# Kernel optimization log

Hardware: AMD Instinct MI355X
Metric: run time of the kernel (lower is better)

The kernel has to match this reference:

```python
import jax, jax.numpy as jnp
import numpy as np

N, E, D, H = 50000, 800000, 128, 4
DH = D // H
BN_EPS = 1e-5


def setup_inputs() -> dict:
    key = jax.random.key(0)
    ks = jax.random.split(key, 16)
    s = 0.02
    inp = {
        "x": jax.random.normal(ks[0], (N, D), dtype=jnp.float32),
        "edge_index": jax.random.randint(ks[1], (2, E), 0, N, dtype=jnp.int64),
        "Wk": jax.random.normal(ks[2], (D, D), dtype=jnp.float32) * s,
        "bk": jnp.zeros((D,), jnp.float32),
        "Wm": jax.random.normal(ks[3], (D, D), dtype=jnp.float32) * s,
        "bm": jnp.zeros((D,), jnp.float32),
        "Wq": jax.random.normal(ks[4], (D, D), dtype=jnp.float32) * s,
        "bq": jnp.zeros((D,), jnp.float32),
        "W1": jax.random.normal(ks[5], (D, D), dtype=jnp.float32) * s,
        "b1": jnp.zeros((D,), jnp.float32),
        "gamma": jnp.ones((D,), jnp.float32),
        "beta": jnp.zeros((D,), jnp.float32),
        "W2": jax.random.normal(ks[6], (D, D), dtype=jnp.float32) * s,
        "b2": jnp.zeros((D,), jnp.float32),
    }
    return inp


def reference(x, edge_index, Wk, bk, Wm, bm, Wq, bq, W1, b1, gamma, beta, W2, b2):
    src = edge_index[0]  # [E] softmax segment key
    dst = edge_index[1]  # [E] aggregation target
    x_i = x[dst]         # [E, D] (torch code: X[1])
    x_j = x[src]         # [E, D] (torch code: X[0])

    key = (x_i @ Wk + bk).reshape(-1, H, DH)
    msg = (x_j @ Wm + bm).reshape(-1, H, DH)
    query = (x_j @ Wq + bq).reshape(-1, H, DH) / jnp.sqrt(jnp.float32(DH))

    scores = jnp.sum(query * key, axis=2)  # [E, H]

    # segment softmax over src node index (numerically stable)
    smax = jax.ops.segment_max(scores, src, num_segments=N)
    e = jnp.exp(scores - smax[src])
    ssum = jax.ops.segment_sum(e, src, num_segments=N)
    alpha = e / ssum[src]  # [E, H]

    # rescale by per-src-node edge count
    cnt = jax.ops.segment_sum(jnp.ones((scores.shape[0],), jnp.float32), src, num_segments=N)
    alpha = alpha * cnt[src][:, None]

    out_e = (msg * alpha[:, :, None]).reshape(-1, D)  # [E, D]
    out = jax.ops.segment_sum(out_e, dst, num_segments=N)  # [N, D]

    # MLP: Linear -> BatchNorm1d (training-mode batch stats) -> ReLU -> Linear
    h = out @ W1 + b1
    mean = jnp.mean(h, axis=0)
    var = jnp.var(h, axis=0)  # biased variance, as torch BN uses for normalization
    h = (h - mean) * jax.lax.rsqrt(var + BN_EPS) * gamma + beta
    h = jax.nn.relu(h)
    return h @ W2 + b2
```

## Files before the change

kernel.cpp:

```cpp
#include <hip/hip_runtime.h>
#include <hip/hip_bf16.h>

#define N_NODES 50000
#define N_EDGES 800000
#define DIM 128
#define NHEAD 4
#define GEMM_BLOCKS 782
#define HBLOCKS 313
#define EPB 2560
#define NBUCK 196
#define NBUCK2 392
#define NODE_PAD 50432

typedef __bf16 bf16x8 __attribute__((ext_vector_type(8)));
typedef float f32x4 __attribute__((ext_vector_type(4)));

struct WPtrs { const float* w[5]; };

__global__ __launch_bounds__(256) void prep_weights(WPtrs P, __bf16* __restrict__ Wt)
{
  __shared__ __bf16 tileT[16][136];
  const int mat = blockIdx.x >> 3, sl = blockIdx.x & 7;
  const float* W = P.w[mat];
  const int col0 = sl * 16;
  const int t = threadIdx.x;
  #pragma unroll
  for (int i = 0; i < 8; ++i) {
    int id = t + i * 256;
    int k = id >> 4, c = id & 15;
    tileT[c][k] = (__bf16)W[k * 128 + col0 + c];
  }
  __syncthreads();
  int c = t >> 4, kb = t & 15;
  bf16x8 v = *(const bf16x8*)&tileT[c][kb * 8];
  *(bf16x8*)&Wt[(size_t)mat * 16384 + (size_t)(col0 + c) * 128 + kb * 8] = v;
}


__device__ __forceinline__ void stage_Wt_half(const __bf16* __restrict__ Wt,
    int half, __bf16 (*wLDS)[136])
{
  const int t = threadIdx.x;
  const __bf16* base = Wt + (size_t)half * 64 * 128;
  #pragma unroll
  for (int i = 0; i < 4; ++i) {
    int id = t + i * 256;
    int col = id >> 4, kb = id & 15;
    bf16x8 v = ((const bf16x8*)(base + (size_t)col * 128))[kb];
    *(bf16x8*)&wLDS[col][kb * 8] = v;
  }
}

__device__ __forceinline__ void stage_A_f32(const float* __restrict__ A, int row0,
    int nrows, __bf16 (*aLDS)[136])
{
  const int t = threadIdx.x;
  #pragma unroll
  for (int i = 0; i < 4; ++i) {
    int id = t + i * 256;
    int r = id >> 4, cb = id & 15;
    int gr = row0 + r;
    float4 v0 = make_float4(0.f, 0.f, 0.f, 0.f), v1 = v0;
    if (gr < nrows) {
      const float4* row = (const float4*)(A + (size_t)gr * DIM);
      v0 = row[cb * 2];
      v1 = row[cb * 2 + 1];
    }
    bf16x8 o;
    o[0] = (__bf16)v0.x; o[1] = (__bf16)v0.y; o[2] = (__bf16)v0.z; o[3] = (__bf16)v0.w;
    o[4] = (__bf16)v1.x; o[5] = (__bf16)v1.y; o[6] = (__bf16)v1.z; o[7] = (__bf16)v1.w;
    *(bf16x8*)&aLDS[r][cb * 8] = o;
  }
}

__device__ __forceinline__ void stage_A_bf16(const __bf16* __restrict__ A, int row0,
    int nrows, __bf16 (*aLDS)[136])
{
  const int t = threadIdx.x;
  #pragma unroll
  for (int i = 0; i < 4; ++i) {
    int id = t + i * 256;
    int r = id >> 4, cb = id & 15;
    int gr = row0 + r;
    bf16x8 v = {};
    if (gr < nrows) v = ((const bf16x8*)(A + (size_t)gr * DIM))[cb];
    *(bf16x8*)&aLDS[r][cb * 8] = v;
  }
}

__device__ __forceinline__ void mfma_half(const __bf16 (*aLDS)[136],
    const __bf16 (*wLDS)[136], int half, f32x4 acc[8])
{
  const int lane = threadIdx.x & 63, wave = threadIdx.x >> 6;
  const int m = lane & 15, q = lane >> 4;
  #pragma unroll
  for (int kt = 0; kt < 4; ++kt) {
    bf16x8 a = *(const bf16x8*)&aLDS[wave * 16 + m][kt * 32 + q * 8];
    #pragma unroll
    for (int ct = 0; ct < 4; ++ct) {
      bf16x8 b = *(const bf16x8*)&wLDS[ct * 16 + m][kt * 32 + q * 8];
      acc[half * 4 + ct] =
          __builtin_amdgcn_mfma_f32_16x16x32_bf16(a, b, acc[half * 4 + ct], 0, 0, 0);
    }
  }
}

template <typename OutT>
__device__ __forceinline__ void store_tile(f32x4 acc[8],
    const float* __restrict__ bias, float scale, OutT* __restrict__ C,
    int row0, int nrows)
{
  const int lane = threadIdx.x & 63, wave = threadIdx.x >> 6;
  const int m = lane & 15, q = lane >> 4;
  #pragma unroll
  for (int j = 0; j < 8; ++j) {
    int col = (j >> 2) * 64 + (j & 3) * 16 + m;
    float bv = bias[col];
    #pragma unroll
    for (int r = 0; r < 4; ++r) {
      int row = row0 + wave * 16 + q * 4 + r;
      if (row < nrows) C[(size_t)row * DIM + col] = (OutT)((acc[j][r] + bv) * scale);
    }
  }
}

__device__ __forceinline__ void gemm_pass(const __bf16 (*aLDS)[136],
    __bf16 (*wLDS)[136], const __bf16* __restrict__ Wt, f32x4 acc[8])
{
  #pragma unroll
  for (int i = 0; i < 8; ++i) acc[i] = (f32x4){0.f, 0.f, 0.f, 0.f};
  stage_Wt_half(Wt, 0, wLDS);
  __syncthreads();
  mfma_half(aLDS, wLDS, 0, acc);
  __syncthreads();
  stage_Wt_half(Wt, 1, wLDS);
  __syncthreads();
  mfma_half(aLDS, wLDS, 1, acc);
}

__global__ __launch_bounds__(256) void fat1(const int* __restrict__ ei,
    int* __restrict__ hist,
    const __bf16* __restrict__ Wt, const float* __restrict__ x,
    const float* __restrict__ bk, const float* __restrict__ bm,
    const float* __restrict__ bq,
    __bf16* __restrict__ Kn, __bf16* __restrict__ Mn, __bf16* __restrict__ Qn)
{
  __shared__ __bf16 aLDS[64][136];
  __shared__ __bf16 wLDS[64][136];
  const int b = blockIdx.x, t = threadIdx.x;

  if (b < HBLOCKS) {
    int* h = (int*)&aLDS[0][0];
    for (int i = t; i < NBUCK2; i += 256) h[i] = 0;
    __syncthreads();
    #pragma unroll
    for (int i = 0; i < 10; ++i) {
      int e = b * EPB + i * 256 + t;
      if (e < N_EDGES) {
        int s = ei[e], d = ei[N_EDGES + e];
        atomicAdd(&h[s >> 8], 1);
        atomicAdd(&h[NBUCK + (d >> 8)], 1);
      }
    }
    __syncthreads();
    for (int i = t; i < NBUCK2; i += 256) hist[b * NBUCK2 + i] = h[i];
  } else {
    const int gb = b - HBLOCKS;
    const int mat = gb % 3;
    const int row0 = (gb / 3) * 64;
    const float* bias = (mat == 0) ? bk : (mat == 1) ? bm : bq;
    __bf16* out = (mat == 0) ? Kn : (mat == 1) ? Mn : Qn;
    const float scale = (mat == 2) ? 0.17677669529663689f : 1.0f;
    f32x4 acc[8];
    stage_A_f32(x, row0, N_NODES, aLDS);
    gemm_pass(aLDS, wLDS, Wt + (size_t)mat * 16384, acc);
    store_tile<__bf16>(acc, bias, scale, out, row0, N_NODES);
  }
}

__global__ __launch_bounds__(64) void bucket_scan(const int* __restrict__ hist,
    int* __restrict__ bbase, int* __restrict__ tot)
{
  const int b = blockIdx.x, l = threadIdx.x;
  int run = 0;
  for (int c = 0; c < 5; ++c) {
    int idx = c * 64 + l;
    int v = (idx < HBLOCKS) ? hist[idx * NBUCK2 + b] : 0;
    int orig = v;
    #pragma unroll
    for (int o = 1; o < 64; o <<= 1) {
      int n = __shfl_up(v, o);
      if (l >= o) v += n;
    }
    if (idx < HBLOCKS) bbase[idx * NBUCK2 + b] = run + v - orig;
    run += __shfl(v, 63);
  }
  if (l == 0) tot[b] = run;
}

__global__ __launch_bounds__(256) void bucket_starts(const int* __restrict__ tot,
    int* __restrict__ bstart)
{
  __shared__ int s[256];
  const int t = threadIdx.x;
  int v = (t < NBUCK) ? tot[t] : 0;
  s[t] = v; __syncthreads();
  for (int o = 1; o < 256; o <<= 1) {
    int x = (t >= o) ? s[t - o] : 0; __syncthreads();
    s[t] += x; __syncthreads();
  }
  if (t < NBUCK) bstart[t] = s[t] - v;
  __syncthreads();
  v = (t < NBUCK) ? tot[NBUCK + t] : 0;
  s[t] = v; __syncthreads();
  for (int o = 1; o < 256; o <<= 1) {
    int x = (t >= o) ? s[t - o] : 0; __syncthreads();
    s[t] += x; __syncthreads();
  }
  if (t < NBUCK) bstart[NBUCK + t] = s[t] - v;
}

__global__ __launch_bounds__(256) void edge_scatter(const int* __restrict__ ei,
    const int* __restrict__ bbase, const int* __restrict__ bstart,
    int2* __restrict__ bucketedS, int* __restrict__ bucketedD)
{
  __shared__ int base[NBUCK2];
  __shared__ int cur[NBUCK2];
  const int b = blockIdx.x, t = threadIdx.x;
  for (int i = t; i < NBUCK2; i += 256) {
    base[i] = bstart[i] + bbase[b * NBUCK2 + i];
    cur[i] = 0;
  }
  __syncthreads();
  #pragma unroll
  for (int i = 0; i < 10; ++i) {
    int e = b * EPB + i * 256 + t;
    if (e < N_EDGES) {
      int s = ei[e], d = ei[N_EDGES + e];
      int pk = s | (d << 16);
      int bs = s >> 8, bd = NBUCK + (d >> 8);
      int lo = atomicAdd(&cur[bs], 1);
      int ld = atomicAdd(&cur[bd], 1);
      int slotD = base[bd] + ld;
      bucketedS[base[bs] + lo] = make_int2(pk, slotD);
      bucketedD[slotD] = pk;
    }
  }
}

__global__ __launch_bounds__(256) void bucket_rank(const int2* __restrict__ bucketedS,
    const int* __restrict__ bucketedD, const int* __restrict__ bstart,
    const int* __restrict__ tot,
    int2* __restrict__ elistS, int* __restrict__ elistD,
    int* __restrict__ starts, int* __restrict__ deg,
    int* __restrict__ startsD, int* __restrict__ degD)
{
  __shared__ int c1[256], ns[256], c2[256];
  const int b = blockIdx.x, t = threadIdx.x;
  const bool srcSide = (b < NBUCK);
  const int bb = srcSide ? b : b - NBUCK;
  const int seg0 = bstart[b];
  const int cnt = tot[b];

  c1[t] = 0; c2[t] = 0;
  __syncthreads();
  if (srcSide) {
    const int2* ent = bucketedS + seg0;
    for (int i = t; i < cnt; i += 256)
      atomicAdd(&c1[(int)((unsigned)ent[i].x & 0xFFFFu) - (bb << 8)], 1);
  } else {
    const int* ent = bucketedD + seg0;
    for (int i = t; i < cnt; i += 256)
      atomicAdd(&c1[(int)((unsigned)ent[i] >> 16) - (bb << 8)], 1);
  }
  __syncthreads();
  ns[t] = c1[t]; __syncthreads();
  for (int o = 1; o < 256; o <<= 1) {
    int x = (t >= o) ? ns[t - o] : 0; __syncthreads();
    ns[t] += x; __syncthreads();
  }
  {
    int node = (bb << 8) + t;
    int st = seg0 + ns[t] - c1[t];
    if (srcSide) { starts[node] = st; deg[node] = c1[t]; }
    else         { startsD[node] = st; degD[node] = c1[t]; }
  }
  __syncthreads();
  ns[t] -= c1[t];
  __syncthreads();
  if (srcSide) {
    const int2* ent = bucketedS + seg0;
    for (int i = t; i < cnt; i += 256) {
      int2 en = ent[i];
      unsigned pk = (unsigned)en.x;
      int ln = (int)(pk & 0xFFFFu) - (bb << 8);
      int r = atomicAdd(&c2[ln], 1);
      elistS[seg0 + ns[ln] + r] = make_int2((int)(pk >> 16), en.y);
    }
  } else {
    const int* ent = bucketedD + seg0;
    for (int i = t; i < cnt; i += 256) {
      unsigned pk = (unsigned)ent[i];
      int ln = (int)(pk >> 16) - (bb << 8);
      int r = atomicAdd(&c2[ln], 1);
      elistD[seg0 + ns[ln] + r] = (int)(pk & 0xFFFFu) | (i << 16);
    }
  }
}

__global__ __launch_bounds__(256) void src_scores(const int* __restrict__ starts,
    const int* __restrict__ degS, const int2* __restrict__ elistS,
    const __bf16* __restrict__ Qn, const __bf16* __restrict__ Kn,
    float* __restrict__ wexp, float* __restrict__ factor)
{
  const int wave = threadIdx.x >> 6, l = threadIdx.x & 63;
  const int n = blockIdx.x * 4 + wave;
  const int g = l >> 4, il = l & 15;
  const int h = il >> 2;
  const int beg = starts[n], end = beg + degS[n];
  if (beg == end) return;

  bf16x8 q8 = ((const bf16x8*)(Qn + (size_t)n * DIM))[il];
  float wsum = 0.f;

  for (int p0 = beg; p0 < end; p0 += 16) {
    int pp[4]; int2 en[4];
    #pragma unroll
    for (int u = 0; u < 4; ++u) {
      pp[u] = p0 + u * 4 + g;
      en[u] = elistS[min(pp[u], end - 1)];
    }
    bf16x8 kk[4];
    #pragma unroll
    for (int u = 0; u < 4; ++u)
      kk[u] = ((const bf16x8*)(Kn + (size_t)en[u].x * DIM))[il];
    #pragma unroll
    for (int u = 0; u < 4; ++u) {
      float pr = 0.f;
      #pragma unroll
      for (int j = 0; j < 8; ++j) pr += (float)q8[j] * (float)kk[u][j];
      pr += __shfl_xor(pr, 1);
      pr += __shfl_xor(pr, 2);
      float w = (pp[u] < end) ? __expf(pr) : 0.f;
      wsum += w;
      if ((pp[u] < end) && (il & 3) == 0) wexp[(size_t)en[u].y * NHEAD + h] = w;
    }
  }
  wsum += __shfl_xor(wsum, 16);
  wsum += __shfl_xor(wsum, 32);
  if (g == 0 && (il & 3) == 0)
    factor[(size_t)n * NHEAD + h] = (float)(end - beg) / wsum;
}

__global__ __launch_bounds__(256) void dst_aggregate(const int* __restrict__ startsD,
    const int* __restrict__ degD, const int* __restrict__ elistD,
    const int* __restrict__ bstart,
    const __bf16* __restrict__ Mn, const float* __restrict__ wexp,
    const float* __restrict__ factor, __bf16* __restrict__ agg)
{
  const int wave = threadIdx.x >> 6, l = threadIdx.x & 63;
  const int n = blockIdx.x * 4 + wave;
  const int g = l >> 4, il = l & 15;
  const int h = il >> 2;
  const int beg = startsD[n], end = beg + degD[n];
  const int seg0d = bstart[NBUCK + (n >> 8)];

  float acc[8];
  #pragma unroll
  for (int j = 0; j < 8; ++j) acc[j] = 0.f;

  for (int q0 = beg; q0 < end; q0 += 16) {
    int qq[4], ss[4]; float ww[4];
    #pragma unroll
    for (int u = 0; u < 4; ++u) {
      qq[u] = q0 + u * 4 + g;
      int cq = min(qq[u], end - 1);
      int v = elistD[cq];
      ss[u] = v & 0xFFFF;
      ww[u] = wexp[(size_t)(seg0d + ((unsigned)v >> 16)) * NHEAD + h];
    }
    float ff[4];
    #pragma unroll
    for (int u = 0; u < 4; ++u) ff[u] = factor[(size_t)ss[u] * NHEAD + h];
    bf16x8 mm[4];
    #pragma unroll
    for (int u = 0; u < 4; ++u)
      mm[u] = ((const bf16x8*)(Mn + (size_t)ss[u] * DIM))[il];
    #pragma unroll
    for (int u = 0; u < 4; ++u) {
      float av = (qq[u] < end) ? ww[u] * ff[u] : 0.f;
      #pragma unroll
      for (int j = 0; j < 8; ++j) acc[j] += (float)mm[u][j] * av;
    }
  }
  #pragma unroll
  for (int j = 0; j < 8; ++j) {
    acc[j] += __shfl_xor(acc[j], 16);
    acc[j] += __shfl_xor(acc[j], 32);
  }
  if (g == 0) {
    bf16x8 o;
    #pragma unroll
    for (int j = 0; j < 8; ++j) o[j] = (__bf16)acc[j];
    *(bf16x8*)(agg + (size_t)n * DIM + il * 8) = o;
  }
}

__global__ __launch_bounds__(256) void gemm_stats(const __bf16* __restrict__ A,
    const __bf16* __restrict__ Wt, const float* __restrict__ bias,
    __bf16* __restrict__ C, float* __restrict__ colsum, float* __restrict__ colsq)
{
  __shared__ __bf16 aLDS[64][136];
  __shared__ __bf16 wLDS[64][136];
  __shared__ float csum[128], csq[128];
  const int t = threadIdx.x;
  const int row0 = blockIdx.x * 64;

  stage_A_bf16(A, row0, N_NODES, aLDS);
  if (t < 128) { csum[t] = 0.f; csq[t] = 0.f; }
  f32x4 acc[8];
  gemm_pass(aLDS, wLDS, Wt, acc);

  const int lane = t & 63, wave = t >> 6;
  const int m = lane & 15, q = lane >> 4;
  #pragma unroll
  for (int j = 0; j < 8; ++j) {
    int col = (j >> 2) * 64 + (j & 3) * 16 + m;
    float bv = bias[col];
    float s = 0.f, s2 = 0.f;
    #pragma unroll
    for (int r = 0; r < 4; ++r) {
      int row = row0 + wave * 16 + q * 4 + r;
      float hv = acc[j][r] + bv;
      if (row < N_NODES) {
        C[(size_t)row * DIM + col] = (__bf16)hv;
        s += hv; s2 += hv * hv;
      }
    }
    s  += __shfl_xor(s, 16);  s  += __shfl_xor(s, 32);
    s2 += __shfl_xor(s2, 16); s2 += __shfl_xor(s2, 32);
    if (q == 0) {
      atomicAdd(&csum[col], s);
      atomicAdd(&csq[col], s2);
    }
  }
  __syncthreads();
  if (t < 128) {
    atomicAdd(&colsum[t], csum[t]);
    atomicAdd(&colsq[t], csq[t]);
  }
}

__global__ __launch_bounds__(256) void gemm_bn(const __bf16* __restrict__ A,
    const __bf16* __restrict__ Wt, const float* __restrict__ bias,
    float* __restrict__ C, const float* __restrict__ colsum,
    const float* __restrict__ colsq, const float* __restrict__ gamma,
    const float* __restrict__ beta)
{
  __shared__ __bf16 aLDS[64][136];
  __shared__ __bf16 wLDS[64][136];
  __shared__ float sA[128], sB[128];
  const int t = threadIdx.x;
  const int row0 = blockIdx.x * 64;

  if (t < 128) {
    float mean = colsum[t] * (1.0f / N_NODES);
    float var = colsq[t] * (1.0f / N_NODES) - mean * mean;
    float inv = rsqrtf(var + 1e-5f);
    float a = gamma[t] * inv;
    sA[t] = a;
    sB[t] = beta[t] - mean * a;
  }
  __syncthreads();

  {
    const int cb = t & 15;
    float sa[8], sb[8];
    #pragma unroll
    for (int j = 0; j < 8; ++j) { sa[j] = sA[cb * 8 + j]; sb[j] = sB[cb * 8 + j]; }
    #pragma unroll
    for (int i = 0; i < 4; ++i) {
      int id = t + i * 256;
      int r = id >> 4;
      int gr = row0 + r;
      bf16x8 v = {};
      if (gr < N_NODES) v = ((const bf16x8*)(A + (size_t)gr * DIM))[cb];
      bf16x8 o;
      #pragma unroll
      for (int j = 0; j < 8; ++j)
        o[j] = (__bf16)fmaxf((float)v[j] * sa[j] + sb[j], 0.f);
      *(bf16x8*)&aLDS[r][cb * 8] = o;
    }
  }
  f32x4 acc[8];
  gemm_pass(aLDS, wLDS, Wt, acc);
  store_tile<float>(acc, bias, 1.0f, C, row0, N_NODES);
}

extern "C" void kernel_launch(void* const* d_in, const int* in_sizes, int n_in,
                              void* d_out, int out_size, void* d_ws, size_t ws_size,
                              hipStream_t stream) {
  const float* x     = (const float*)d_in[0];
  const int*   ei    = (const int*)d_in[1];
  const float* Wk    = (const float*)d_in[2];
  const float* bk    = (const float*)d_in[3];
  const float* Wm    = (const float*)d_in[4];
  const float* bm    = (const float*)d_in[5];
  const float* Wq    = (const float*)d_in[6];
  const float* bq    = (const float*)d_in[7];
  const float* W1    = (const float*)d_in[8];
  const float* b1    = (const float*)d_in[9];
  const float* gamma = (const float*)d_in[10];
  const float* beta  = (const float*)d_in[11];
  const float* W2    = (const float*)d_in[12];
  const float* b2    = (const float*)d_in[13];

  float* ws = (float*)d_ws;
  const size_t ND  = (size_t)N_NODES * DIM;
  const size_t NDh = ND / 2;
  const size_t EH  = (size_t)N_EDGES * NHEAD;

  __bf16* Kn   = (__bf16*)ws;
  __bf16* Mn   = (__bf16*)(ws + NDh);
  __bf16* Qn   = (__bf16*)(ws + 2 * NDh);
  __bf16* agg  = (__bf16*)(ws + 3 * NDh);
  __bf16* h1   = (__bf16*)(ws + 4 * NDh);
  float*  wexp = ws + 5 * NDh;
  int2*   bucketedS = (int2*)wexp;
  int*    bucketedD = (int*)(bucketedS + N_EDGES);
  int2*   elistS = (int2*)(wexp + EH);
  int*    elistD = (int*)(elistS + N_EDGES);
  int*    hist   = elistD + N_EDGES;
  int*    bbase  = hist + HBLOCKS * NBUCK2;
  int*    tot    = bbase + HBLOCKS * NBUCK2;
  int*    bstart = tot + NBUCK2;
  int*    starts = bstart + NBUCK2;
  int*    deg    = starts + NODE_PAD;
  int*    startsD= deg + NODE_PAD;
  int*    degD   = startsD + NODE_PAD;
  float*  factor = (float*)(degD + NODE_PAD);
  float*  colsum = factor + (size_t)NHEAD * N_NODES;
  float*  colsq  = colsum + 128;
  __bf16* Wt     = (__bf16*)(colsq + 128);
  float*  outp   = (float*)d_out;

  hipMemsetAsync(colsum, 0, 256 * sizeof(float), stream);

  const int node_blocks = N_NODES / 4;

  WPtrs wp; wp.w[0] = Wk; wp.w[1] = Wm; wp.w[2] = Wq; wp.w[3] = W1; wp.w[4] = W2;
  prep_weights<<<40, 256, 0, stream>>>(wp, Wt);

  fat1<<<HBLOCKS + 3 * GEMM_BLOCKS, 256, 0, stream>>>(
      ei, hist, Wt, x, bk, bm, bq, Kn, Mn, Qn);

  bucket_scan<<<NBUCK2, 64, 0, stream>>>(hist, bbase, tot);
  bucket_starts<<<1, 256, 0, stream>>>(tot, bstart);
  edge_scatter<<<HBLOCKS, 256, 0, stream>>>(ei, bbase, bstart, bucketedS, bucketedD);
  bucket_rank<<<NBUCK2, 256, 0, stream>>>(bucketedS, bucketedD, bstart, tot,
                                          elistS, elistD, starts, deg,
                                          startsD, degD);

  src_scores<<<node_blocks, 256, 0, stream>>>(starts, deg, elistS, Qn, Kn,
                                              wexp, factor);
  dst_aggregate<<<node_blocks, 256, 0, stream>>>(startsD, degD, elistD, bstart,
                                                 Mn, wexp, factor, agg);

  gemm_stats<<<GEMM_BLOCKS, 256, 0, stream>>>(agg, Wt + 3 * 16384, b1, h1,
                                              colsum, colsq);
  gemm_bn<<<GEMM_BLOCKS, 256, 0, stream>>>(h1, Wt + 4 * 16384, b2, outp,
                                           colsum, colsq, gamma, beta);
}
```

Baseline: 290.8 us.

## Store K/M/Q and agg head-major and assign one wave per node-head

```diff
diff --git a/kernel.cpp b/kernel.cpp
--- a/kernel.cpp
+++ b/kernel.cpp
@@ -5,6 +5,7 @@
 #define N_EDGES 800000
 #define DIM 128
 #define NHEAD 4
+#define HN (N_NODES * 32)
 #define GEMM_BLOCKS 782
 #define HBLOCKS 313
 #define EPB 2560
@@ -73,7 +74,7 @@
   }
 }
 
-__device__ __forceinline__ void stage_A_bf16(const __bf16* __restrict__ A, int row0,
+__device__ __forceinline__ void stage_A_hm(const __bf16* __restrict__ A, int row0,
     int nrows, __bf16 (*aLDS)[136])
 {
   const int t = threadIdx.x;
@@ -83,7 +84,8 @@
     int r = id >> 4, cb = id & 15;
     int gr = row0 + r;
     bf16x8 v = {};
-    if (gr < nrows) v = ((const bf16x8*)(A + (size_t)gr * DIM))[cb];
+    if (gr < nrows)
+      v = *(const bf16x8*)(A + (size_t)(cb >> 2) * HN + (size_t)gr * 32 + (cb & 3) * 8);
     *(bf16x8*)&aLDS[r][cb * 8] = v;
   }
 }
@@ -120,6 +122,25 @@
     for (int r = 0; r < 4; ++r) {
       int row = row0 + wave * 16 + q * 4 + r;
       if (row < nrows) C[(size_t)row * DIM + col] = (OutT)((acc[j][r] + bv) * scale);
+    }
+  }
+}
+
+__device__ __forceinline__ void store_tile_hm(f32x4 acc[8],
+    const float* __restrict__ bias, float scale, __bf16* __restrict__ C,
+    int row0, int nrows)
+{
+  const int lane = threadIdx.x & 63, wave = threadIdx.x >> 6;
+  const int m = lane & 15, q = lane >> 4;
+  #pragma unroll
+  for (int j = 0; j < 8; ++j) {
+    int col = (j >> 2) * 64 + (j & 3) * 16 + m;
+    float bv = bias[col];
+    __bf16* base = C + (size_t)(col >> 5) * HN + (col & 31);
+    #pragma unroll
+    for (int r = 0; r < 4; ++r) {
+      int row = row0 + wave * 16 + q * 4 + r;
+      if (row < nrows) base[(size_t)row * 32] = (__bf16)((acc[j][r] + bv) * scale);
     }
   }
 }
@@ -174,7 +195,7 @@
     f32x4 acc[8];
     stage_A_f32(x, row0, N_NODES, aLDS);
     gemm_pass(aLDS, wLDS, Wt + (size_t)mat * 16384, acc);
-    store_tile<__bf16>(acc, bias, scale, out, row0, N_NODES);
+    store_tile_hm(acc, bias, scale, out, row0, N_NODES);
   }
 }
 
@@ -310,91 +331,74 @@
 
 __global__ __launch_bounds__(256) void src_scores(const int* __restrict__ starts,
     const int* __restrict__ degS, const int2* __restrict__ elistS,
-    const __bf16* __restrict__ Qn, const __bf16* __restrict__ Kn,
+    const __bf16* __restrict__ Qh, const __bf16* __restrict__ Kh,
     float* __restrict__ wexp, float* __restrict__ factor)
 {
-  const int wave = threadIdx.x >> 6, l = threadIdx.x & 63;
-  const int n = blockIdx.x * 4 + wave;
-  const int g = l >> 4, il = l & 15;
-  const int h = il >> 2;
+  const int wid = blockIdx.x * 4 + (threadIdx.x >> 6);
+  const int l = threadIdx.x & 63;
+  const int n = wid >> 2, h = wid & 3;
+  const int g = l >> 2, il = l & 3;
   const int beg = starts[n], end = beg + degS[n];
   if (beg == end) return;
 
-  bf16x8 q8 = ((const bf16x8*)(Qn + (size_t)n * DIM))[il];
+  const __bf16* Kb = Kh + (size_t)h * HN;
+  bf16x8 q8 = ((const bf16x8*)(Qh + (size_t)h * HN + (size_t)n * 32))[il];
   float wsum = 0.f;
 
   for (int p0 = beg; p0 < end; p0 += 16) {
-    int pp[4]; int2 en[4];
-    #pragma unroll
-    for (int u = 0; u < 4; ++u) {
-      pp[u] = p0 + u * 4 + g;
-      en[u] = elistS[min(pp[u], end - 1)];
-    }
-    bf16x8 kk[4];
-    #pragma unroll
-    for (int u = 0; u < 4; ++u)
-      kk[u] = ((const bf16x8*)(Kn + (size_t)en[u].x * DIM))[il];
-    #pragma unroll
-    for (int u = 0; u < 4; ++u) {
-      float pr = 0.f;
-      #pragma unroll
-      for (int j = 0; j < 8; ++j) pr += (float)q8[j] * (float)kk[u][j];
-      pr += __shfl_xor(pr, 1);
-      pr += __shfl_xor(pr, 2);
-      float w = (pp[u] < end) ? __expf(pr) : 0.f;
-      wsum += w;
-      if ((pp[u] < end) && (il & 3) == 0) wexp[(size_t)en[u].y * NHEAD + h] = w;
-    }
-  }
+    int p = p0 + g;
+    int2 en = elistS[min(p, end - 1)];
+    bf16x8 kk = ((const bf16x8*)(Kb + (size_t)en.x * 32))[il];
+    float pr = 0.f;
+    #pragma unroll
+    for (int j = 0; j < 8; ++j) pr += (float)q8[j] * (float)kk[j];
+    pr += __shfl_xor(pr, 1);
+    pr += __shfl_xor(pr, 2);
+    float w = (p < end) ? __expf(pr) : 0.f;
+    wsum += w;
+    if ((p < end) && il == 0) wexp[(size_t)en.y * NHEAD + h] = w;
+  }
+  wsum += __shfl_xor(wsum, 4);
+  wsum += __shfl_xor(wsum, 8);
   wsum += __shfl_xor(wsum, 16);
   wsum += __shfl_xor(wsum, 32);
-  if (g == 0 && (il & 3) == 0)
-    factor[(size_t)n * NHEAD + h] = (float)(end - beg) / wsum;
+  if (l == 0) factor[(size_t)n * NHEAD + h] = (float)(end - beg) / wsum;
 }
 
 __global__ __launch_bounds__(256) void dst_aggregate(const int* __restrict__ startsD,
     const int* __restrict__ degD, const int* __restrict__ elistD,
     const int* __restrict__ bstart,
-    const __bf16* __restrict__ Mn, const float* __restrict__ wexp,
+    const __bf16* __restrict__ Mh, const float* __restrict__ wexp,
     const float* __restrict__ factor, __bf16* __restrict__ agg)
 {
-  const int wave = threadIdx.x >> 6, l = threadIdx.x & 63;
-  const int n = blockIdx.x * 4 + wave;
-  const int g = l >> 4, il = l & 15;
-  const int h = il >> 2;
+  const int wid = blockIdx.x * 4 + (threadIdx.x >> 6);
+  const int l = threadIdx.x & 63;
+  const int n = wid >> 2, h = wid & 3;
+  const int g = l >> 2, il = l & 3;
   const int beg = startsD[n], end = beg + degD[n];
   const int seg0d = bstart[NBUCK + (n >> 8)];
+  const __bf16* Mb = Mh + (size_t)h * HN;
 
   float acc[8];
   #pragma unroll
   for (int j = 0; j < 8; ++j) acc[j] = 0.f;
 
-  for (int q0 = beg; q0 < end; q0 += 16) {
-    int qq[4], ss[4]; float ww[4];
-    #pragma unroll
-    for (int u = 0; u < 4; ++u) {
-      qq[u] = q0 + u * 4 + g;
-      int cq = min(qq[u], end - 1);
-      int v = elistD[cq];
-      ss[u] = v & 0xFFFF;
-      ww[u] = wexp[(size_t)(seg0d + ((unsigned)v >> 16)) * NHEAD + h];
-    }
-    float ff[4];
-    #pragma unroll
-    for (int u = 0; u < 4; ++u) ff[u] = factor[(size_t)ss[u] * NHEAD + h];
-    bf16x8 mm[4];
-    #pragma unroll
-    for (int u = 0; u < 4; ++u)
-      mm[u] = ((const bf16x8*)(Mn + (size_t)ss[u] * DIM))[il];
-    #pragma unroll
-    for (int u = 0; u < 4; ++u) {
-      float av = (qq[u] < end) ? ww[u] * ff[u] : 0.f;
-      #pragma unroll
-      for (int j = 0; j < 8; ++j) acc[j] += (float)mm[u][j] * av;
-    }
+  for (int p0 = beg; p0 < end; p0 += 16) {
+    int p = p0 + g;
+    int cq = min(p, end - 1);
+    int v = elistD[cq];
+    int src = v & 0xFFFF;
+    float w = wexp[(size_t)(seg0d + ((unsigned)v >> 16)) * NHEAD + h]
+            * factor[src * NHEAD + h];
+    bf16x8 mm = ((const bf16x8*)(Mb + (size_t)src * 32))[il];
+    float av = (p < end) ? w : 0.f;
+    #pragma unroll
+    for (int j = 0; j < 8; ++j) acc[j] += (float)mm[j] * av;
   }
   #pragma unroll
   for (int j = 0; j < 8; ++j) {
+    acc[j] += __shfl_xor(acc[j], 4);
+    acc[j] += __shfl_xor(acc[j], 8);
     acc[j] += __shfl_xor(acc[j], 16);
     acc[j] += __shfl_xor(acc[j], 32);
   }
@@ -402,7 +406,7 @@
     bf16x8 o;
     #pragma unroll
     for (int j = 0; j < 8; ++j) o[j] = (__bf16)acc[j];
-    *(bf16x8*)(agg + (size_t)n * DIM + il * 8) = o;
+    *(bf16x8*)(agg + (size_t)h * HN + (size_t)n * 32 + il * 8) = o;
   }
 }
 
@@ -416,7 +420,7 @@
   const int t = threadIdx.x;
   const int row0 = blockIdx.x * 64;
 
-  stage_A_bf16(A, row0, N_NODES, aLDS);
+  stage_A_hm(A, row0, N_NODES, aLDS);
   if (t < 128) { csum[t] = 0.f; csq[t] = 0.f; }
   f32x4 acc[8];
   gemm_pass(aLDS, wLDS, Wt, acc);
@@ -546,7 +550,7 @@
 
   hipMemsetAsync(colsum, 0, 256 * sizeof(float), stream);
 
-  const int node_blocks = N_NODES / 4;
+  const int nh_blocks = N_NODES;
 
   WPtrs wp; wp.w[0] = Wk; wp.w[1] = Wm; wp.w[2] = Wq; wp.w[3] = W1; wp.w[4] = W2;
   prep_weights<<<40, 256, 0, stream>>>(wp, Wt);
@@ -561,10 +565,10 @@
                                           elistS, elistD, starts, deg,
                                           startsD, degD);
 
-  src_scores<<<node_blocks, 256, 0, stream>>>(starts, deg, elistS, Qn, Kn,
-                                              wexp, factor);
-  dst_aggregate<<<node_blocks, 256, 0, stream>>>(startsD, degD, elistD, bstart,
-                                                 Mn, wexp, factor, agg);
+  src_scores<<<nh_blocks, 256, 0, stream>>>(starts, deg, elistS, Qn, Kn,
+                                            wexp, factor);
+  dst_aggregate<<<nh_blocks, 256, 0, stream>>>(startsD, degD, elistD, bstart,
+                                               Mn, wexp, factor, agg);
 
   gemm_stats<<<GEMM_BLOCKS, 256, 0, stream>>>(agg, Wt + 3 * 16384, b1, h1,
                                               colsum, colsq);
```

Measured after the change: 367.8 us. 26.5% more time.

## Read GEMM weights directly from global memory and fuse K/M/Q projections per tile

Applied to the files above, without the earlier changes.

```diff
diff --git a/kernel.cpp b/kernel.cpp
--- a/kernel.cpp
+++ b/kernel.cpp
@@ -37,20 +37,6 @@
 }
 
 
-__device__ __forceinline__ void stage_Wt_half(const __bf16* __restrict__ Wt,
-    int half, __bf16 (*wLDS)[136])
-{
-  const int t = threadIdx.x;
-  const __bf16* base = Wt + (size_t)half * 64 * 128;
-  #pragma unroll
-  for (int i = 0; i < 4; ++i) {
-    int id = t + i * 256;
-    int col = id >> 4, kb = id & 15;
-    bf16x8 v = ((const bf16x8*)(base + (size_t)col * 128))[kb];
-    *(bf16x8*)&wLDS[col][kb * 8] = v;
-  }
-}
-
 __device__ __forceinline__ void stage_A_f32(const float* __restrict__ A, int row0,
     int nrows, __bf16 (*aLDS)[136])
 {
@@ -88,19 +74,21 @@
   }
 }
 
-__device__ __forceinline__ void mfma_half(const __bf16 (*aLDS)[136],
-    const __bf16 (*wLDS)[136], int half, f32x4 acc[8])
+__device__ __forceinline__ void gemm_direct(const __bf16 (*aLDS)[136],
+    const __bf16* __restrict__ Wt, f32x4 acc[8])
 {
   const int lane = threadIdx.x & 63, wave = threadIdx.x >> 6;
   const int m = lane & 15, q = lane >> 4;
   #pragma unroll
+  for (int i = 0; i < 8; ++i) acc[i] = (f32x4){0.f, 0.f, 0.f, 0.f};
+  #pragma unroll
   for (int kt = 0; kt < 4; ++kt) {
     bf16x8 a = *(const bf16x8*)&aLDS[wave * 16 + m][kt * 32 + q * 8];
     #pragma unroll
-    for (int ct = 0; ct < 4; ++ct) {
-      bf16x8 b = *(const bf16x8*)&wLDS[ct * 16 + m][kt * 32 + q * 8];
-      acc[half * 4 + ct] =
-          __builtin_amdgcn_mfma_f32_16x16x32_bf16(a, b, acc[half * 4 + ct], 0, 0, 0);
+    for (int j = 0; j < 8; ++j) {
+      int col = (j >> 2) * 64 + (j & 3) * 16 + m;
+      bf16x8 b = *(const bf16x8*)&Wt[(size_t)col * 128 + kt * 32 + q * 8];
+      acc[j] = __builtin_amdgcn_mfma_f32_16x16x32_bf16(a, b, acc[j], 0, 0, 0);
     }
   }
 }
@@ -122,20 +110,6 @@
       if (row < nrows) C[(size_t)row * DIM + col] = (OutT)((acc[j][r] + bv) * scale);
     }
   }
-}
-
-__device__ __forceinline__ void gemm_pass(const __bf16 (*aLDS)[136],
-    __bf16 (*wLDS)[136], const __bf16* __restrict__ Wt, f32x4 acc[8])
-{
-  #pragma unroll
-  for (int i = 0; i < 8; ++i) acc[i] = (f32x4){0.f, 0.f, 0.f, 0.f};
-  stage_Wt_half(Wt, 0, wLDS);
-  __syncthreads();
-  mfma_half(aLDS, wLDS, 0, acc);
-  __syncthreads();
-  stage_Wt_half(Wt, 1, wLDS);
-  __syncthreads();
-  mfma_half(aLDS, wLDS, 1, acc);
 }
 
 __global__ __launch_bounds__(256) void fat1(const int* __restrict__ ei,
@@ -146,7 +120,6 @@
     __bf16* __restrict__ Kn, __bf16* __restrict__ Mn, __bf16* __restrict__ Qn)
 {
   __shared__ __bf16 aLDS[64][136];
-  __shared__ __bf16 wLDS[64][136];
   const int b = blockIdx.x, t = threadIdx.x;
 
   if (b < HBLOCKS) {
@@ -165,16 +138,16 @@
     __syncthreads();
     for (int i = t; i < NBUCK2; i += 256) hist[b * NBUCK2 + i] = h[i];
   } else {
-    const int gb = b - HBLOCKS;
-    const int mat = gb % 3;
-    const int row0 = (gb / 3) * 64;
-    const float* bias = (mat == 0) ? bk : (mat == 1) ? bm : bq;
-    __bf16* out = (mat == 0) ? Kn : (mat == 1) ? Mn : Qn;
-    const float scale = (mat == 2) ? 0.17677669529663689f : 1.0f;
+    const int row0 = (b - HBLOCKS) * 64;
     f32x4 acc[8];
     stage_A_f32(x, row0, N_NODES, aLDS);
-    gemm_pass(aLDS, wLDS, Wt + (size_t)mat * 16384, acc);
-    store_tile<__bf16>(acc, bias, scale, out, row0, N_NODES);
+    __syncthreads();
+    gemm_direct(aLDS, Wt, acc);
+    store_tile<__bf16>(acc, bk, 1.0f, Kn, row0, N_NODES);
+    gemm_direct(aLDS, Wt + 16384, acc);
+    store_tile<__bf16>(acc, bm, 1.0f, Mn, row0, N_NODES);
+    gemm_direct(aLDS, Wt + 32768, acc);
+    store_tile<__bf16>(acc, bq, 0.17677669529663689f, Qn, row0, N_NODES);
   }
 }
 
@@ -411,15 +384,15 @@
     __bf16* __restrict__ C, float* __restrict__ colsum, float* __restrict__ colsq)
 {
   __shared__ __bf16 aLDS[64][136];
-  __shared__ __bf16 wLDS[64][136];
   __shared__ float csum[128], csq[128];
   const int t = threadIdx.x;
   const int row0 = blockIdx.x * 64;
 
   stage_A_bf16(A, row0, N_NODES, aLDS);
   if (t < 128) { csum[t] = 0.f; csq[t] = 0.f; }
+  __syncthreads();
   f32x4 acc[8];
-  gemm_pass(aLDS, wLDS, Wt, acc);
+  gemm_direct(aLDS, Wt, acc);
 
   const int lane = t & 63, wave = t >> 6;
   const int m = lane & 15, q = lane >> 4;
@@ -458,7 +431,6 @@
     const float* __restrict__ beta)
 {
   __shared__ __bf16 aLDS[64][136];
-  __shared__ __bf16 wLDS[64][136];
   __shared__ float sA[128], sB[128];
   const int t = threadIdx.x;
   const int row0 = blockIdx.x * 64;
@@ -492,8 +464,9 @@
       *(bf16x8*)&aLDS[r][cb * 8] = o;
     }
   }
+  __syncthreads();
   f32x4 acc[8];
-  gemm_pass(aLDS, wLDS, Wt, acc);
+  gemm_direct(aLDS, Wt, acc);
   store_tile<float>(acc, bias, 1.0f, C, row0, N_NODES);
 }
 
@@ -551,7 +524,7 @@
   WPtrs wp; wp.w[0] = Wk; wp.w[1] = Wm; wp.w[2] = Wq; wp.w[3] = W1; wp.w[4] = W2;
   prep_weights<<<40, 256, 0, stream>>>(wp, Wt);
 
-  fat1<<<HBLOCKS + 3 * GEMM_BLOCKS, 256, 0, stream>>>(
+  fat1<<<HBLOCKS + GEMM_BLOCKS, 256, 0, stream>>>(
       ei, hist, Wt, x, bk, bm, bq, Kn, Mn, Qn);
 
   bucket_scan<<<NBUCK2, 64, 0, stream>>>(hist, bbase, tot);
```

New measurement: 336.8 us. 1.16x slower.

## Reuse staged x tile across K/M/Q GEMMs and compress src edge list

Applied to the files above, without the earlier changes.

```diff
diff --git a/kernel.cpp b/kernel.cpp
--- a/kernel.cpp
+++ b/kernel.cpp
@@ -165,16 +165,17 @@
     __syncthreads();
     for (int i = t; i < NBUCK2; i += 256) hist[b * NBUCK2 + i] = h[i];
   } else {
-    const int gb = b - HBLOCKS;
-    const int mat = gb % 3;
-    const int row0 = (gb / 3) * 64;
-    const float* bias = (mat == 0) ? bk : (mat == 1) ? bm : bq;
-    __bf16* out = (mat == 0) ? Kn : (mat == 1) ? Mn : Qn;
-    const float scale = (mat == 2) ? 0.17677669529663689f : 1.0f;
+    const int row0 = (b - HBLOCKS) * 64;
     f32x4 acc[8];
     stage_A_f32(x, row0, N_NODES, aLDS);
-    gemm_pass(aLDS, wLDS, Wt + (size_t)mat * 16384, acc);
-    store_tile<__bf16>(acc, bias, scale, out, row0, N_NODES);
+    gemm_pass(aLDS, wLDS, Wt, acc);
+    store_tile<__bf16>(acc, bk, 1.0f, Kn, row0, N_NODES);
+    __syncthreads();
+    gemm_pass(aLDS, wLDS, Wt + 16384, acc);
+    store_tile<__bf16>(acc, bm, 1.0f, Mn, row0, N_NODES);
+    __syncthreads();
+    gemm_pass(aLDS, wLDS, Wt + 32768, acc);
+    store_tile<__bf16>(acc, bq, 0.17677669529663689f, Qn, row0, N_NODES);
   }
 }
 
@@ -251,7 +252,7 @@
 __global__ __launch_bounds__(256) void bucket_rank(const int2* __restrict__ bucketedS,
     const int* __restrict__ bucketedD, const int* __restrict__ bstart,
     const int* __restrict__ tot,
-    int2* __restrict__ elistS, int* __restrict__ elistD,
+    int* __restrict__ elistS, int* __restrict__ elistD,
     int* __restrict__ starts, int* __restrict__ deg,
     int* __restrict__ startsD, int* __restrict__ degD)
 {
@@ -293,9 +294,11 @@
     for (int i = t; i < cnt; i += 256) {
       int2 en = ent[i];
       unsigned pk = (unsigned)en.x;
+      int dstn = (int)(pk >> 16);
       int ln = (int)(pk & 0xFFFFu) - (bb << 8);
       int r = atomicAdd(&c2[ln], 1);
-      elistS[seg0 + ns[ln] + r] = make_int2((int)(pk >> 16), en.y);
+      int local = en.y - bstart[NBUCK + (dstn >> 8)];
+      elistS[seg0 + ns[ln] + r] = dstn | (local << 16);
     }
   } else {
     const int* ent = bucketedD + seg0;
@@ -309,7 +312,8 @@
 }
 
 __global__ __launch_bounds__(256) void src_scores(const int* __restrict__ starts,
-    const int* __restrict__ degS, const int2* __restrict__ elistS,
+    const int* __restrict__ degS, const int* __restrict__ elistS,
+    const int* __restrict__ bstart,
     const __bf16* __restrict__ Qn, const __bf16* __restrict__ Kn,
     float* __restrict__ wexp, float* __restrict__ factor)
 {
@@ -324,16 +328,16 @@
   float wsum = 0.f;
 
   for (int p0 = beg; p0 < end; p0 += 16) {
-    int pp[4]; int2 en[4];
+    int pp[4]; unsigned en[4];
     #pragma unroll
     for (int u = 0; u < 4; ++u) {
       pp[u] = p0 + u * 4 + g;
-      en[u] = elistS[min(pp[u], end - 1)];
+      en[u] = (unsigned)elistS[min(pp[u], end - 1)];
     }
     bf16x8 kk[4];
     #pragma unroll
     for (int u = 0; u < 4; ++u)
-      kk[u] = ((const bf16x8*)(Kn + (size_t)en[u].x * DIM))[il];
+      kk[u] = ((const bf16x8*)(Kn + (size_t)(en[u] & 0xFFFFu) * DIM))[il];
     #pragma unroll
     for (int u = 0; u < 4; ++u) {
       float pr = 0.f;
@@ -343,7 +347,11 @@
       pr += __shfl_xor(pr, 2);
       float w = (pp[u] < end) ? __expf(pr) : 0.f;
       wsum += w;
-      if ((pp[u] < end) && (il & 3) == 0) wexp[(size_t)en[u].y * NHEAD + h] = w;
+      if ((pp[u] < end) && (il & 3) == 0) {
+        int dstn = (int)(en[u] & 0xFFFFu);
+        int slot = bstart[NBUCK + (dstn >> 8)] + (int)(en[u] >> 16);
+        wexp[(size_t)slot * NHEAD + h] = w;
+      }
     }
   }
   wsum += __shfl_xor(wsum, 16);
@@ -528,8 +536,8 @@
   float*  wexp = ws + 5 * NDh;
   int2*   bucketedS = (int2*)wexp;
   int*    bucketedD = (int*)(bucketedS + N_EDGES);
-  int2*   elistS = (int2*)(wexp + EH);
-  int*    elistD = (int*)(elistS + N_EDGES);
+  int*    elistS = (int*)(wexp + EH);
+  int*    elistD = elistS + N_EDGES;
   int*    hist   = elistD + N_EDGES;
   int*    bbase  = hist + HBLOCKS * NBUCK2;
   int*    tot    = bbase + HBLOCKS * NBUCK2;
@@ -551,7 +559,7 @@
   WPtrs wp; wp.w[0] = Wk; wp.w[1] = Wm; wp.w[2] = Wq; wp.w[3] = W1; wp.w[4] = W2;
   prep_weights<<<40, 256, 0, stream>>>(wp, Wt);
 
-  fat1<<<HBLOCKS + 3 * GEMM_BLOCKS, 256, 0, stream>>>(
+  fat1<<<HBLOCKS + GEMM_BLOCKS, 256, 0, stream>>>(
       ei, hist, Wt, x, bk, bm, bq, Kn, Mn, Qn);
 
   bucket_scan<<<NBUCK2, 64, 0, stream>>>(hist, bbase, tot);
@@ -561,8 +569,8 @@
                                           elistS, elistD, starts, deg,
                                           startsD, degD);
 
-  src_scores<<<node_blocks, 256, 0, stream>>>(starts, deg, elistS, Qn, Kn,
-                                              wexp, factor);
+  src_scores<<<node_blocks, 256, 0, stream>>>(starts, deg, elistS, bstart,
+                                              Qn, Kn, wexp, factor);
   dst_aggregate<<<node_blocks, 256, 0, stream>>>(startsD, degD, elistD, bstart,
                                                  Mn, wexp, factor, agg);
 
```

Result: no change. 291.7 us (+0.3%).
